# Optimization experiments

Measured on AMD Instinct MI355X. Metric: run time of the kernel, lower is better.

The kernel has to match this reference:

```python
import jax, jax.numpy as jnp
import numpy as np

EPS_DIST = 1e-7  # matches torch: log((d+1)/(d+1e-7))


def _cdist(x, p):
    # x: (B, N, D), p: (P, D) -> (B, N, P) Euclidean distances
    x2 = jnp.sum(x * x, axis=-1, keepdims=True)        # (B, N, 1)
    p2 = jnp.sum(p * p, axis=-1)                       # (P,)
    d2 = x2 + p2[None, None, :] - 2.0 * jnp.einsum('bnd,pd->bnp', x, p)
    return jnp.sqrt(jnp.maximum(d2, 1e-12))


def setup_inputs() -> dict:
    key = jax.random.key(0)
    k1, k2, k3 = jax.random.split(key, 3)
    B, C, H, W = 32, 2048, 14, 14
    num_classes, npc = 200, 10
    P = num_classes * npc
    x = jax.random.normal(k1, (B, C, H, W), dtype=jnp.float32)
    prototypes = jax.random.normal(k2, (1, P, C), dtype=jnp.float32)
    fc_w = jax.random.normal(k3, (num_classes, P), dtype=jnp.float32) * 0.02
    return {"x": x, "prototypes": prototypes, "fc_w": fc_w}


def reference(x, prototypes, fc_w):
    B, C, H, W = x.shape
    feats = x.reshape(B, C, H * W).transpose(0, 2, 1)   # (B, HW, D)
    protos = prototypes[0]                              # (P, D)
    num_classes = fc_w.shape[0]
    npc = protos.shape[0] // num_classes

    distances = _cdist(feats, protos)                   # (B, HW, P)
    similarity = jnp.log((distances + 1.0) / (distances + EPS_DIST))
    max_similarity = jnp.max(similarity, axis=1)        # (B, P)
    min_distances = jnp.min(distances, axis=1)          # (B, P)
    min_distances_per_class = min_distances.reshape(B, num_classes, npc)
    scores = max_similarity @ fc_w.T                    # (B, num_classes)
    return scores, min_distances_per_class
```

## Files before the change

### kernel.cpp

```cpp
#include <hip/hip_runtime.h>

#define INF_BITS 0x7F800000u
#define AS1 __attribute__((address_space(1)))
#define AS3 __attribute__((address_space(3)))

typedef float f32x4 __attribute__((ext_vector_type(4)));
typedef int i32x4 __attribute__((ext_vector_type(4)));
typedef int i32x8 __attribute__((ext_vector_type(8)));
typedef unsigned int u32x2 __attribute__((ext_vector_type(2)));
typedef unsigned int u32x4 __attribute__((ext_vector_type(4)));

template <int SEL>
static __device__ __forceinline__ float dq8(unsigned int w) {
  return __builtin_amdgcn_cvt_f32_fp8((int)w, SEL);
}

__global__ __launch_bounds__(256) void k_prep_p(const float* __restrict__ protos,
                                                unsigned char* __restrict__ pTf,
                                                float* __restrict__ p2,
                                                unsigned int* __restrict__ outu) {
  const int row = blockIdx.x;
  const int tid = threadIdx.x;
  const int gi = row * 256 + tid;
  if (gi < 64000) outu[6400 + gi] = INF_BITS;
  __shared__ float red[4];
  float s = 0.f;
  unsigned int w0 = 0u, w1 = 0u;
  if (row < 2000) {
    const float* src = protos + (size_t)row * 2048 + tid * 8;
    f32x4 a = *(const f32x4*)src;
    f32x4 c = *(const f32x4*)(src + 4);
    w0 = (unsigned int)__builtin_amdgcn_cvt_pk_fp8_f32(a.x, a.y, 0, false);
    w0 = (unsigned int)__builtin_amdgcn_cvt_pk_fp8_f32(a.z, a.w, (int)w0, true);
    w1 = (unsigned int)__builtin_amdgcn_cvt_pk_fp8_f32(c.x, c.y, 0, false);
    w1 = (unsigned int)__builtin_amdgcn_cvt_pk_fp8_f32(c.z, c.w, (int)w1, true);
    float q;
    q = dq8<0>(w0); s += q * q;
    q = dq8<1>(w0); s += q * q;
    q = dq8<2>(w0); s += q * q;
    q = dq8<3>(w0); s += q * q;
    q = dq8<0>(w1); s += q * q;
    q = dq8<1>(w1); s += q * q;
    q = dq8<2>(w1); s += q * q;
    q = dq8<3>(w1); s += q * q;
  }
  *(u32x2*)(pTf + (size_t)row * 2048 + tid * 8) = (u32x2){w0, w1};
  #pragma unroll
  for (int off = 32; off; off >>= 1) s += __shfl_xor(s, off);
  if ((tid & 63) == 0) red[tid >> 6] = s;
  __syncthreads();
  if (tid == 0) p2[row] = red[0] + red[1] + red[2] + red[3];
}

__global__ __launch_bounds__(256) void k_prep_x(const float* __restrict__ x,
                                                unsigned char* __restrict__ xTf,
                                                float* __restrict__ x2p,
                                                float* __restrict__ x2) {
  const int kt = blockIdx.x;
  const int b  = blockIdx.y;
  const int tid = threadIdx.x;
  if (b == 32) {
    u32x4* pad = (u32x4*)(xTf + (size_t)6272 * 2048);
    #pragma unroll
    for (int j = tid; j < 512; j += 256)
      pad[kt * 512 + j] = (u32x4){0u, 0u, 0u, 0u};
    if (kt == 0 && tid < 128) x2[6272 + tid] = __uint_as_float(INF_BITS);
    return;
  }
  __shared__ unsigned char Ls[64][208];
  const float* src = x + ((size_t)b * 2048 + (size_t)kt * 64) * 196;
  for (int idx = tid; idx < 3136; idx += 256) {
    const int kk = idx / 49, c4 = idx - kk * 49;
    f32x4 v = *(const f32x4*)(src + (size_t)kk * 196 + c4 * 4);
    unsigned int w = (unsigned int)__builtin_amdgcn_cvt_pk_fp8_f32(v.x, v.y, 0, false);
    w = (unsigned int)__builtin_amdgcn_cvt_pk_fp8_f32(v.z, v.w, (int)w, true);
    *(unsigned int*)&Ls[kk][c4 * 4] = w;
  }
  __syncthreads();
  if (tid < 196) {
    float s = 0.f;
    #pragma unroll
    for (int j = 0; j < 64; ++j) {
      float v = dq8<0>((unsigned int)Ls[j][tid]);
      s += v * v;
    }
    x2p[kt * 6272 + b * 196 + tid] = s;
  }
  unsigned char* dstb = xTf + (size_t)b * 196 * 2048 + kt * 64;
  for (int idx = tid; idx < 784; idx += 256) {
    const int n = idx >> 2, q = idx & 3;
    const int k0 = q * 16;
    u32x4 v;
    #pragma unroll
    for (int j = 0; j < 4; ++j) {
      v[j] = (unsigned int)Ls[k0 + 4 * j + 0][n] |
             ((unsigned int)Ls[k0 + 4 * j + 1][n] << 8) |
             ((unsigned int)Ls[k0 + 4 * j + 2][n] << 16) |
             ((unsigned int)Ls[k0 + 4 * j + 3][n] << 24);
    }
    *(u32x4*)(dstb + (size_t)n * 2048 + k0) = v;
  }
}

__global__ void k_x2r(const float* __restrict__ x2p, float* __restrict__ x2) {
  int i = blockIdx.x * blockDim.x + threadIdx.x;
  if (i >= 6272) return;
  float s = 0.f;
  #pragma unroll
  for (int c = 0; c < 32; ++c) s += x2p[c * 6272 + i];
  x2[i] = s;
}

__global__ __launch_bounds__(512, 2) void k_main(
    const unsigned char* __restrict__ pTf, const unsigned char* __restrict__ xTf,
    const float* __restrict__ p2, const float* __restrict__ x2,
    unsigned int* __restrict__ outu) {
  const int orig = blockIdx.x;
  const int wgid = (orig & 7) * 25 + (orig >> 3);
  const int ptpair = wgid / 50;
  const int rem = wgid - ptpair * 50;
  const int ptile = ptpair * 2 + (rem & 1);
  const int mtile = rem >> 1;
  const int p0 = ptile * 256;
  const int m0 = mtile * 256;
  const int tid = threadIdx.x;
  const int lane = tid & 63;
  const int w = tid >> 6;
  const int wp = w >> 2;
  const int wn = w & 3;
  const int lr = lane & 15;
  const int lg = lane >> 4;

  __shared__ __align__(16) char S[131072];

  f32x4 acc[8][4];
  #pragma unroll
  for (int mi = 0; mi < 8; ++mi)
    #pragma unroll
    for (int ni = 0; ni < 4; ++ni)
      acc[mi][ni] = (f32x4){0.f, 0.f, 0.f, 0.f};

  const int rowbase = tid >> 3;
  const int chunk = (tid & 7) ^ (rowbase & 7);
  const char* gA = (const char*)pTf + (size_t)(p0 + rowbase) * 2048 + chunk * 16;
  const char* gB = (const char*)xTf + (size_t)(m0 + rowbase) * 2048 + chunk * 16;
  const int wbase = w * 1024;

#define STAGE_A(c_, kt_, h_) do {                                              \
    const char* s_ = gA + (size_t)((h_) * 128 * 2048) + (size_t)(kt_) * 128;   \
    _Pragma("unroll")                                                          \
    for (int j_ = 0; j_ < 2; ++j_)                                             \
      __builtin_amdgcn_global_load_lds(                                        \
          (const AS1 void*)(s_ + (size_t)j_ * 64 * 2048),                      \
          (AS3 void*)(S + (c_) * 32768 + (h_) * 16384 + j_ * 8192 + wbase),    \
          16, 0, 0);                                                           \
  } while (0)
#define STAGE_B(c_, kt_, h_) do {                                              \
    const char* s_ = gB + (size_t)((h_) * 128 * 2048) + (size_t)(kt_) * 128;   \
    _Pragma("unroll")                                                          \
    for (int j_ = 0; j_ < 2; ++j_)                                             \
      __builtin_amdgcn_global_load_lds(                                        \
          (const AS1 void*)(s_ + (size_t)j_ * 64 * 2048),                      \
          (AS3 void*)(S + 65536 + (c_) * 32768 + (h_) * 16384 + j_ * 8192 + wbase), \
          16, 0, 0);                                                           \
  } while (0)

  const int swz = ((lr & 7) << 4);
  const int koffA = (lg * 32) ^ swz;
  const int arow = (wp * 128 + lr) * 128;
  const int brow = (wn * 64 + lr) * 128;

#define READ_A1(dst_, c_, a_) do {                                             \
    const char* p_ = S + (c_) * 32768 + arow + (a_) * 2048;                    \
    u32x4 lo_ = *(const u32x4*)(p_ + koffA);                                   \
    u32x4 hi_ = *(const u32x4*)(p_ + (koffA ^ 16));                            \
    dst_ = __builtin_bit_cast(i32x8,                                           \
        __builtin_shufflevector(lo_, hi_, 0, 1, 2, 3, 4, 5, 6, 7));            \
  } while (0)
#define READ_B4(dst_, c_)                                                      \
    _Pragma("unroll")                                                          \
    for (int ni_ = 0; ni_ < 4; ++ni_) {                                        \
      const char* p_ = S + 65536 + (c_) * 32768 + brow + ni_ * 2048;           \
      u32x4 lo_ = *(const u32x4*)(p_ + koffA);                                 \
      u32x4 hi_ = *(const u32x4*)(p_ + (koffA ^ 16));                          \
      dst_[ni_] = __builtin_bit_cast(i32x8,                                    \
          __builtin_shufflevector(lo_, hi_, 0, 1, 2, 3, 4, 5, 6, 7));          \
    }

#define SCHED() __builtin_amdgcn_sched_barrier(0)
#define SBAR() do { SCHED(); __builtin_amdgcn_s_barrier(); SCHED(); } while (0)
#define LGKM0() do { asm volatile("s_waitcnt lgkmcnt(0)" ::: "memory"); SCHED(); } while (0)
#define MFMA4(mi_, af_, bf_) do { __builtin_amdgcn_s_setprio(1);               \
    _Pragma("unroll")                                                          \
    for (int ni_ = 0; ni_ < 4; ++ni_)                                          \
      acc[mi_][ni_] = __builtin_amdgcn_mfma_scale_f32_16x16x128_f8f6f4(        \
          af_, bf_[ni_], acc[mi_][ni_], 0, 0, 0, 0x7F7F7F7F, 0, 0x7F7F7F7F);   \
    __builtin_amdgcn_s_setprio(0); } while (0)

#define KT_BODY(kt_, c_, sa_, sb_, vm_, tail_) do {                            \
    if (sa_) { STAGE_A((c_) ^ 1, (kt_) + 1, 0); STAGE_A((c_) ^ 1, (kt_) + 1, 1); } \
    i32x8 bf[4], af0, af1;                                                     \
    READ_B4(bf, c_);                                                           \
    READ_A1(af0, c_, 0);                                                       \
    READ_A1(af1, c_, 1); MFMA4(0, af0, bf); SCHED();                           \
    READ_A1(af0, c_, 2); MFMA4(1, af1, bf); SCHED();                           \
    READ_A1(af1, c_, 3); MFMA4(2, af0, bf); SCHED();                           \
    READ_A1(af0, c_, 4); MFMA4(3, af1, bf); SCHED();                           \
    READ_A1(af1, c_, 5); MFMA4(4, af0, bf); SCHED();                           \
    READ_A1(af0, c_, 6); MFMA4(5, af1, bf); SCHED();                           \
    READ_A1(af1, c_, 7); MFMA4(6, af0, bf); SCHED();                           \
    MFMA4(7, af1, bf);                                                         \
    if (!(tail_)) {                                                            \
      LGKM0();                                                                 \
      SBAR();                                               \
      if (sb_) { STAGE_B(c_, (kt_) + 2, 0); STAGE_B(c_, (kt_) + 2, 1); }       \
      if ((vm_) == 4)      asm volatile("s_waitcnt vmcnt(4)" ::: "memory");    \
      else if ((vm_) == 0) asm volatile("s_waitcnt vmcnt(0)" ::: "memory");    \
      SCHED();                                                                 \
      SBAR();                                             \
    }                                                                          \
  } while (0)

  STAGE_A(0, 0, 0); STAGE_A(0, 0, 1);
  STAGE_B(0, 0, 0); STAGE_B(0, 0, 1);
  STAGE_B(1, 1, 0); STAGE_B(1, 1, 1);
  asm volatile("s_waitcnt vmcnt(4)" ::: "memory");
  SCHED();
  __builtin_amdgcn_s_barrier();
  SCHED();

  #pragma unroll 1
  for (int it = 0; it < 7; ++it) {
    KT_BODY(2 * it, 0, 1, 1, 4, 0);
    KT_BODY(2 * it + 1, 1, 1, 1, 4, 0);
  }
  KT_BODY(14, 0, 1, 0, 0, 0);
  KT_BODY(15, 1, 0, 0, -1, 1);
#undef KT_BODY
#undef MFMA4
#undef READ_A1
#undef READ_B4
#undef STAGE_A
#undef STAGE_B

  const int wm_base = m0 + wn * 64;
  const int b_lo = wm_base / 196;
  int b_hi = (wm_base + 63) / 196;
  if (b_hi > 31) b_hi = 31;
  const bool wave_ok = (b_lo < 32);
  float x2v[4];
  int seg0[4];
  #pragma unroll
  for (int ni = 0; ni < 4; ++ni) {
    const int m = wm_base + ni * 16 + lr;
    x2v[ni] = x2[m];
    seg0[ni] = ((m / 196) == b_lo);
  }
  const float INF = __uint_as_float(INF_BITS);
  #pragma unroll
  for (int mi = 0; mi < 8; ++mi) {
    const int prow = p0 + wp * 128 + mi * 16 + 4 * lg;
    #pragma unroll
    for (int j = 0; j < 4; ++j) {
      const int p = prow + j;
      const float pp = p2[p];
      float ma = INF, mb = INF;
      #pragma unroll
      for (int ni = 0; ni < 4; ++ni) {
        const float d2 = x2v[ni] + pp - 2.f * acc[mi][ni][j];
        ma = fminf(ma, seg0[ni] ? d2 : INF);
        mb = fminf(mb, seg0[ni] ? INF : d2);
      }
      #pragma unroll
      for (int off = 1; off < 16; off <<= 1) {
        ma = fminf(ma, __shfl_xor(ma, off));
        mb = fminf(mb, __shfl_xor(mb, off));
      }
      if (lr == 0 && p < 2000 && wave_ok) {
        atomicMin(&outu[6400 + b_lo * 2000 + p], __float_as_uint(fmaxf(ma, 0.f)));
        if (b_hi != b_lo)
          atomicMin(&outu[6400 + b_hi * 2000 + p], __float_as_uint(fmaxf(mb, 0.f)));
      }
    }
  }
}

__global__ void k_post(float* __restrict__ out, float* __restrict__ simbuf) {
  int i = blockIdx.x * blockDim.x + threadIdx.x;
  if (i >= 64000) return;
  float d2 = out[6400 + i];
  float d = sqrtf(fmaxf(d2, 1e-12f));
  out[6400 + i] = d;
  simbuf[i] = logf((d + 1.0f) / (d + 1e-7f));
}

__global__ __launch_bounds__(256) void k_scores(const float* __restrict__ fc_w,
                                                const float* __restrict__ simbuf,
                                                float* __restrict__ out) {
  const int id = blockIdx.x * 4 + (threadIdx.x >> 6);
  const int lane = threadIdx.x & 63;
  const int b = id / 200;
  const int c = id - b * 200;
  const f32x4* sv = (const f32x4*)(simbuf + (size_t)b * 2000);
  const f32x4* wv = (const f32x4*)(fc_w + (size_t)c * 2000);
  float s = 0.f;
  #pragma unroll
  for (int it = 0; it < 8; ++it) {
    int i = lane + it * 64;
    if (i < 500) {
      f32x4 a = sv[i], w4 = wv[i];
      s += a.x * w4.x + a.y * w4.y + a.z * w4.z + a.w * w4.w;
    }
  }
  #pragma unroll
  for (int off = 32; off; off >>= 1) s += __shfl_xor(s, off);
  if (lane == 0) out[b * 200 + c] = s;
}

extern "C" void kernel_launch(void* const* d_in, const int* in_sizes, int n_in,
                              void* d_out, int out_size, void* d_ws, size_t ws_size,
                              hipStream_t stream) {
  const float* x      = (const float*)d_in[0];
  const float* protos = (const float*)d_in[1];
  const float* fc_w   = (const float*)d_in[2];
  float* out = (float*)d_out;

  char* wsb = (char*)d_ws;
  unsigned char* pTf = (unsigned char*)wsb;
  unsigned char* xTf = (unsigned char*)(wsb + 4194304);
  float* p2   = (float*)(wsb + 17301504);
  float* x2   = (float*)(wsb + 17309696);
  float* x2p  = (float*)(wsb + 17335296);
  float* simb = (float*)(wsb + 17335296);

  k_prep_p<<<2048, 256, 0, stream>>>(protos, pTf, p2, (unsigned int*)d_out);
  k_prep_x<<<dim3(32, 33), 256, 0, stream>>>(x, xTf, x2p, x2);
  k_x2r<<<25, 256, 0, stream>>>(x2p, x2);
  k_main<<<200, 512, 0, stream>>>(pTf, xTf, p2, x2, (unsigned int*)d_out);
  k_post<<<250, 256, 0, stream>>>(out, simb);
  k_scores<<<1600, 256, 0, stream>>>(fc_w, simb, out);
}
```

Before: 83.56 us.

## Shrink main GEMM tile to 256x128 and launch 400 workgroups

Changes the fp8 MFMA distance kernel from 256x256 output tiles with 200 workgroups to 256x128 tiles with 400 workgroups. The wave layout becomes 4x2 with 64x64 per wave, and staging, LDS sizes and vmcnt waits are rewritten to match. The goal is to fill all compute units on the 256-CU MI355X, since 200 workgroups left many idle, and to lower LDS use to 96KB. In exchange, each tile reuses less data, so more prototype data is loaded per output, and the epilogue issues more atomic min updates.

```diff
diff --git a/kernel.cpp b/kernel.cpp
--- a/kernel.cpp
+++ b/kernel.cpp
@@ -5,7 +5,6 @@
 #define AS3 __attribute__((address_space(3)))
 
 typedef float f32x4 __attribute__((ext_vector_type(4)));
-typedef int i32x4 __attribute__((ext_vector_type(4)));
 typedef int i32x8 __attribute__((ext_vector_type(8)));
 typedef unsigned int u32x2 __attribute__((ext_vector_type(2)));
 typedef unsigned int u32x4 __attribute__((ext_vector_type(4)));
@@ -116,26 +115,24 @@
     const float* __restrict__ p2, const float* __restrict__ x2,
     unsigned int* __restrict__ outu) {
   const int orig = blockIdx.x;
-  const int wgid = (orig & 7) * 25 + (orig >> 3);
-  const int ptpair = wgid / 50;
-  const int rem = wgid - ptpair * 50;
-  const int ptile = ptpair * 2 + (rem & 1);
-  const int mtile = rem >> 1;
+  const int wgid = (orig & 7) * 50 + (orig >> 3);
+  const int ptile = wgid / 50;
+  const int mtile = wgid - ptile * 50;
   const int p0 = ptile * 256;
-  const int m0 = mtile * 256;
+  const int m0 = mtile * 128;
   const int tid = threadIdx.x;
   const int lane = tid & 63;
   const int w = tid >> 6;
-  const int wp = w >> 2;
-  const int wn = w & 3;
+  const int wp = w >> 1;
+  const int wn = w & 1;
   const int lr = lane & 15;
   const int lg = lane >> 4;
 
-  __shared__ __align__(16) char S[131072];
-
-  f32x4 acc[8][4];
-  #pragma unroll
-  for (int mi = 0; mi < 8; ++mi)
+  __shared__ __align__(16) char S[98304];
+
+  f32x4 acc[4][4];
+  #pragma unroll
+  for (int mi = 0; mi < 4; ++mi)
     #pragma unroll
     for (int ni = 0; ni < 4; ++ni)
       acc[mi][ni] = (f32x4){0.f, 0.f, 0.f, 0.f};
@@ -146,28 +143,26 @@
   const char* gB = (const char*)xTf + (size_t)(m0 + rowbase) * 2048 + chunk * 16;
   const int wbase = w * 1024;
 
-#define STAGE_A(c_, kt_, h_) do {                                              \
-    const char* s_ = gA + (size_t)((h_) * 128 * 2048) + (size_t)(kt_) * 128;   \
+#define STAGE_A(c_, kt_) do {                                                  \
+    const char* s_ = gA + (size_t)(kt_) * 128;                                 \
+    _Pragma("unroll")                                                          \
+    for (int j_ = 0; j_ < 4; ++j_)                                             \
+      __builtin_amdgcn_global_load_lds(                                        \
+          (const AS1 void*)(s_ + (size_t)j_ * 64 * 2048),                      \
+          (AS3 void*)(S + (c_) * 32768 + j_ * 8192 + wbase), 16, 0, 0);        \
+  } while (0)
+#define STAGE_B(c_, kt_) do {                                                  \
+    const char* s_ = gB + (size_t)(kt_) * 128;                                 \
     _Pragma("unroll")                                                          \
     for (int j_ = 0; j_ < 2; ++j_)                                             \
       __builtin_amdgcn_global_load_lds(                                        \
           (const AS1 void*)(s_ + (size_t)j_ * 64 * 2048),                      \
-          (AS3 void*)(S + (c_) * 32768 + (h_) * 16384 + j_ * 8192 + wbase),    \
-          16, 0, 0);                                                           \
-  } while (0)
-#define STAGE_B(c_, kt_, h_) do {                                              \
-    const char* s_ = gB + (size_t)((h_) * 128 * 2048) + (size_t)(kt_) * 128;   \
-    _Pragma("unroll")                                                          \
-    for (int j_ = 0; j_ < 2; ++j_)                                             \
-      __builtin_amdgcn_global_load_lds(                                        \
-          (const AS1 void*)(s_ + (size_t)j_ * 64 * 2048),                      \
-          (AS3 void*)(S + 65536 + (c_) * 32768 + (h_) * 16384 + j_ * 8192 + wbase), \
-          16, 0, 0);                                                           \
+          (AS3 void*)(S + 65536 + (c_) * 16384 + j_ * 8192 + wbase), 16, 0, 0);\
   } while (0)
 
   const int swz = ((lr & 7) << 4);
   const int koffA = (lg * 32) ^ swz;
-  const int arow = (wp * 128 + lr) * 128;
+  const int arow = (wp * 64 + lr) * 128;
   const int brow = (wn * 64 + lr) * 128;
 
 #define READ_A1(dst_, c_, a_) do {                                             \
@@ -180,7 +175,7 @@
 #define READ_B4(dst_, c_)                                                      \
     _Pragma("unroll")                                                          \
     for (int ni_ = 0; ni_ < 4; ++ni_) {                                        \
-      const char* p_ = S + 65536 + (c_) * 32768 + brow + ni_ * 2048;           \
+      const char* p_ = S + 65536 + (c_) * 16384 + brow + ni_ * 2048;           \
       u32x4 lo_ = *(const u32x4*)(p_ + koffA);                                 \
       u32x4 hi_ = *(const u32x4*)(p_ + (koffA ^ 16));                          \
       dst_[ni_] = __builtin_bit_cast(i32x8,                                    \
@@ -198,41 +193,37 @@
     __builtin_amdgcn_s_setprio(0); } while (0)
 
 #define KT_BODY(kt_, c_, sa_, sb_, vm_, tail_) do {                            \
-    if (sa_) { STAGE_A((c_) ^ 1, (kt_) + 1, 0); STAGE_A((c_) ^ 1, (kt_) + 1, 1); } \
+    if (sa_) STAGE_A((c_) ^ 1, (kt_) + 1);                                     \
     i32x8 bf[4], af0, af1;                                                     \
     READ_B4(bf, c_);                                                           \
     READ_A1(af0, c_, 0);                                                       \
     READ_A1(af1, c_, 1); MFMA4(0, af0, bf); SCHED();                           \
     READ_A1(af0, c_, 2); MFMA4(1, af1, bf); SCHED();                           \
     READ_A1(af1, c_, 3); MFMA4(2, af0, bf); SCHED();                           \
-    READ_A1(af0, c_, 4); MFMA4(3, af1, bf); SCHED();                           \
-    READ_A1(af1, c_, 5); MFMA4(4, af0, bf); SCHED();                           \
-    READ_A1(af0, c_, 6); MFMA4(5, af1, bf); SCHED();                           \
-    READ_A1(af1, c_, 7); MFMA4(6, af0, bf); SCHED();                           \
-    MFMA4(7, af1, bf);                                                         \
+    MFMA4(3, af1, bf);                                                         \
     if (!(tail_)) {                                                            \
       LGKM0();                                                                 \
       SBAR();                                               \
-      if (sb_) { STAGE_B(c_, (kt_) + 2, 0); STAGE_B(c_, (kt_) + 2, 1); }       \
-      if ((vm_) == 4)      asm volatile("s_waitcnt vmcnt(4)" ::: "memory");    \
+      if (sb_) STAGE_B(c_, (kt_) + 2);                                         \
+      if ((vm_) == 2)      asm volatile("s_waitcnt vmcnt(2)" ::: "memory");    \
       else if ((vm_) == 0) asm volatile("s_waitcnt vmcnt(0)" ::: "memory");    \
       SCHED();                                                                 \
       SBAR();                                             \
     }                                                                          \
   } while (0)
 
-  STAGE_A(0, 0, 0); STAGE_A(0, 0, 1);
-  STAGE_B(0, 0, 0); STAGE_B(0, 0, 1);
-  STAGE_B(1, 1, 0); STAGE_B(1, 1, 1);
-  asm volatile("s_waitcnt vmcnt(4)" ::: "memory");
+  STAGE_A(0, 0);
+  STAGE_B(0, 0);
+  STAGE_B(1, 1);
+  asm volatile("s_waitcnt vmcnt(2)" ::: "memory");
   SCHED();
   __builtin_amdgcn_s_barrier();
   SCHED();
 
   #pragma unroll 1
   for (int it = 0; it < 7; ++it) {
-    KT_BODY(2 * it, 0, 1, 1, 4, 0);
-    KT_BODY(2 * it + 1, 1, 1, 1, 4, 0);
+    KT_BODY(2 * it, 0, 1, 1, 2, 0);
+    KT_BODY(2 * it + 1, 1, 1, 1, 2, 0);
   }
   KT_BODY(14, 0, 1, 0, 0, 0);
   KT_BODY(15, 1, 0, 0, -1, 1);
@@ -258,8 +249,8 @@
   }
   const float INF = __uint_as_float(INF_BITS);
   #pragma unroll
-  for (int mi = 0; mi < 8; ++mi) {
-    const int prow = p0 + wp * 128 + mi * 16 + 4 * lg;
+  for (int mi = 0; mi < 4; ++mi) {
+    const int prow = p0 + wp * 64 + mi * 16 + 4 * lg;
     #pragma unroll
     for (int j = 0; j < 4; ++j) {
       const int p = prow + j;
@@ -336,7 +327,7 @@
   k_prep_p<<<2048, 256, 0, stream>>>(protos, pTf, p2, (unsigned int*)d_out);
   k_prep_x<<<dim3(32, 33), 256, 0, stream>>>(x, xTf, x2p, x2);
   k_x2r<<<25, 256, 0, stream>>>(x2p, x2);
-  k_main<<<200, 512, 0, stream>>>(pTf, xTf, p2, x2, (unsigned int*)d_out);
+  k_main<<<400, 512, 0, stream>>>(pTf, xTf, p2, x2, (unsigned int*)d_out);
   k_post<<<250, 256, 0, stream>>>(out, simb);
   k_scores<<<1600, 256, 0, stream>>>(fc_w, simb, out);
 }
```

New measurement: 83.36 us (median of 3 runs). Within noise of the previous version (-0.2%).
